# Optimization experiments

Measured on AMD Instinct MI355X. Metric: run time of the kernel, lower is better.

Reference implementation:

```python
import jax, jax.numpy as jnp
import numpy as np

NUM_HEADS = 8
EPS = 1e-12  # matches torch F.normalize eps


def setup_inputs() -> dict:
    key = jax.random.key(0)
    ks = jax.random.split(key, 4)
    B, C, H, W = 32, 384, 32, 32
    x = jax.random.normal(ks[0], (B, C, H, W), dtype=jnp.float32)
    w_qkv = jax.random.normal(ks[1], (3 * C, C), dtype=jnp.float32) * (1.0 / np.sqrt(C))
    b_qkv = jnp.zeros((3 * C,), dtype=jnp.float32)
    temperature = jnp.ones((NUM_HEADS, 1, 1), dtype=jnp.float32)
    w_proj = jax.random.normal(ks[2], (C, C), dtype=jnp.float32) * (1.0 / np.sqrt(C))
    b_proj = jnp.zeros((C,), dtype=jnp.float32)
    return {"x": x, "w_qkv": w_qkv, "b_qkv": b_qkv, "temperature": temperature,
            "w_proj": w_proj, "b_proj": b_proj}


def _l2norm_tokens(t):
    # L2-normalize over the token axis N (last dim), torch F.normalize semantics
    n = jnp.sqrt(jnp.sum(t * t, axis=-1, keepdims=True))
    return t / jnp.maximum(n, EPS)


def reference(x, w_qkv, b_qkv, temperature, w_proj, b_proj):
    B, C, H, W = x.shape
    N = H * W
    nh = NUM_HEADS
    dh = C // nh
    xf = x.reshape(B, C, N)
    # 1x1 conv == channel GEMM: [B,3C,N]
    qkv = jnp.einsum('oc,bcn->bon', w_qkv, xf) + b_qkv[:, None]
    qkv = qkv.reshape(B, 3, nh, dh, N)
    q, k, v = qkv[:, 0], qkv[:, 1], qkv[:, 2]  # each [B,nh,dh,N]
    q = _l2norm_tokens(q)
    k = _l2norm_tokens(k)
    # cross-covariance: contract over N -> small [B,nh,dh,dh]
    attn = jnp.einsum('bhdn,bhen->bhde', q, k) * temperature
    attn = jax.nn.softmax(attn, axis=-1)
    out = jnp.einsum('bhde,bhen->bhdn', attn, v).reshape(B, C, N)
    out = jnp.einsum('oc,bcn->bon', w_proj, out) + b_proj[:, None]
    return x + out.reshape(B, C, H, W)
```

## Files before the change

kernel.cpp:

```cpp
#include <hip/hip_runtime.h>
#include <hip/hip_bf16.h>
#include <stdint.h>

#define BATCH  32
#define CDIM   384
#define NTOK   1024
#define NHEADS 8
#define DH     48

using f32x4  = __attribute__((ext_vector_type(4))) float;
using bf16x8 = __attribute__((ext_vector_type(8))) short;
using u16x4  = __attribute__((ext_vector_type(4))) uint16_t;
using u16x8  = __attribute__((ext_vector_type(8))) uint16_t;

__device__ __forceinline__ uint16_t f2bf(float f) {
  uint32_t x = __float_as_uint(f);
  uint32_t r = (x + 0x7fffu + ((x >> 16) & 1u)) >> 16;
  return (uint16_t)r;
}
__device__ __forceinline__ float bf2f(uint16_t u) {
  return __uint_as_float(((uint32_t)u) << 16);
}

#define GLL16(gsrc, ldst)                                                    \
  __builtin_amdgcn_global_load_lds(                                          \
      (const __attribute__((address_space(1))) void*)(gsrc),                 \
      (__attribute__((address_space(3))) void*)(ldst), 16, 0, 0)

__global__ __launch_bounds__(256) void k_transpose_x(const float* __restrict__ x,
                                                     uint16_t* __restrict__ xT) {
  __shared__ float t[64][65];
  int tid = threadIdx.x;
  int n0 = blockIdx.x * 64;
  int c0 = blockIdx.y * 64;
  int b  = blockIdx.z;
  const float* xb = x + (size_t)b * CDIM * NTOK;
#pragma unroll
  for (int p = 0; p < 4; ++p) {
    int r  = (tid >> 4) + p * 16;
    int cc = (tid & 15) * 4;
    float4 v = *(const float4*)(xb + (size_t)(c0 + r) * NTOK + n0 + cc);
    t[r][cc + 0] = v.x; t[r][cc + 1] = v.y; t[r][cc + 2] = v.z; t[r][cc + 3] = v.w;
  }
  __syncthreads();
  uint16_t* xTb = xT + (size_t)b * NTOK * CDIM;
#pragma unroll
  for (int p = 0; p < 2; ++p) {
    int n  = (tid >> 3) + p * 32;
    int cb = (tid & 7) * 8;
    u16x8 o;
#pragma unroll
    for (int j = 0; j < 8; ++j) o[j] = f2bf(t[cb + j][n]);
    *(u16x8*)(xTb + (size_t)(n0 + n) * CDIM + c0 + cb) = o;
  }
}

__global__ __launch_bounds__(256) void k_convert_w(const float* __restrict__ wqkv,
                                                   const float* __restrict__ wproj,
                                                   uint16_t* __restrict__ wq,
                                                   uint16_t* __restrict__ wp) {
  int n1 = 3 * CDIM * CDIM;
  int n2 = CDIM * CDIM;
  int stride = gridDim.x * 256;
  for (int i = blockIdx.x * 256 + threadIdx.x; i < n1 + n2; i += stride) {
    if (i < n1) wq[i] = f2bf(wqkv[i]);
    else        wp[i - n1] = f2bf(wproj[i - n1]);
  }
}

__device__ __forceinline__ void gemm_tile_128(const uint16_t* __restrict__ A,
                                              const uint16_t* __restrict__ B,
                                              uint16_t* ldsA, uint16_t* ldsB,
                                              f32x4 acc[4][4], int tid) {
  const int K = 384;
  int w = tid >> 6, lane = tid & 63;
  int wr = w >> 1, wc = w & 1;
  int lr = lane & 15, g = lane >> 4;
  for (int kt = 0; kt < K; kt += 64) {
    __syncthreads();
#pragma unroll
    for (int iss = 0; iss < 4; ++iss) {
      int ch = tid + 256 * iss;
      int r  = ch >> 3;
      int cs = (((ch & 7) ^ (r & 7)) << 3);
      GLL16(A + (size_t)r * K + kt + cs, ldsA + (size_t)ch * 8);
      GLL16(B + (size_t)r * K + kt + cs, ldsB + (size_t)ch * 8);
    }
    __syncthreads();
#pragma unroll
    for (int ks = 0; ks < 2; ++ks) {
      bf16x8 af[4], bfr[4];
#pragma unroll
      for (int mt = 0; mt < 4; ++mt) {
        int row = wr * 64 + mt * 16 + lr;
        int sl  = (((ks * 4 + g) ^ (row & 7)) << 3);
        af[mt] = *(const bf16x8*)(ldsA + (size_t)row * 64 + sl);
      }
#pragma unroll
      for (int nt = 0; nt < 4; ++nt) {
        int row = wc * 64 + nt * 16 + lr;
        int sl  = (((ks * 4 + g) ^ (row & 7)) << 3);
        bfr[nt] = *(const bf16x8*)(ldsB + (size_t)row * 64 + sl);
      }
#pragma unroll
      for (int mt = 0; mt < 4; ++mt)
#pragma unroll
        for (int nt = 0; nt < 4; ++nt)
          acc[mt][nt] = __builtin_amdgcn_mfma_f32_16x16x32_bf16(af[mt], bfr[nt], acc[mt][nt], 0, 0, 0);
    }
  }
}

__global__ __launch_bounds__(256) void k_qkv(const uint16_t* __restrict__ Wq,
                                             const uint16_t* __restrict__ xT,
                                             const float* __restrict__ bqkv,
                                             uint16_t* __restrict__ qk,
                                             uint16_t* __restrict__ vT) {
  __shared__ uint16_t ldsA[128 * 64];
  __shared__ uint16_t ldsB[128 * 64];
  int tid = threadIdx.x;
  int id  = blockIdx.x;
  int xcd = id & 7, idx = id >> 3;
  int jt  = xcd * 32 + (idx & 31);
  int bm  = idx >> 5;
  int o0 = bm * 128, j0 = jt * 128;
  f32x4 acc[4][4];
#pragma unroll
  for (int i = 0; i < 4; ++i)
#pragma unroll
    for (int j = 0; j < 4; ++j) acc[i][j] = (f32x4){0.f, 0.f, 0.f, 0.f};

  gemm_tile_128(Wq + (size_t)o0 * 384, xT + (size_t)j0 * 384, ldsA, ldsB, acc, tid);

  int w = tid >> 6, lane = tid & 63;
  int wr = w >> 1, wc = w & 1, lr = lane & 15, g = lane >> 4;
#pragma unroll
  for (int mt = 0; mt < 4; ++mt) {
    int ob = o0 + wr * 64 + mt * 16 + g * 4;
    float b0 = bqkv[ob + 0], b1 = bqkv[ob + 1], b2 = bqkv[ob + 2], b3 = bqkv[ob + 3];
#pragma unroll
    for (int nt = 0; nt < 4; ++nt) {
      int j = j0 + wc * 64 + nt * 16 + lr;
      int b = j >> 10, n = j & 1023;
      f32x4 v = acc[mt][nt];
      float v0 = v[0] + b0, v1 = v[1] + b1, v2 = v[2] + b2, v3 = v[3] + b3;
      if (ob < 768) {
        uint16_t* dst = qk + ((size_t)(b * 768 + ob) * 1024 + n);
        dst[0] = f2bf(v0); dst[1024] = f2bf(v1); dst[2048] = f2bf(v2); dst[3072] = f2bf(v3);
      } else {
        int oc = ob - 768;
        int h = oc / 48, d = oc % 48;
        u16x4 p;
        p[0] = f2bf(v0); p[1] = f2bf(v1); p[2] = f2bf(v2); p[3] = f2bf(v3);
        *(u16x4*)(vT + ((size_t)((b * 8 + h) * 1024 + n) * 48 + d)) = p;
      }
    }
  }
}

__global__ __launch_bounds__(256) void k_attn(const uint16_t* __restrict__ qk,
                                              const uint16_t* __restrict__ vT,
                                              const float* __restrict__ temperature,
                                              uint16_t* __restrict__ aT) {
  __shared__ float Sp[4][48][49];
  __shared__ float Sf[48][49];
  __shared__ uint16_t P[48][72];
  __shared__ float nrm[96];
  int tid = threadIdx.x, w = tid >> 6, lane = tid & 63;
  int bh = blockIdx.x, b = bh >> 3, h = bh & 7;
  const uint16_t* qbase = qk + (size_t)(b * 768 + h * 48) * 1024;
  const uint16_t* kbase = qbase + (size_t)384 * 1024;

  for (int r = w; r < 96; r += 4) {
    const uint16_t* row = (r < 48) ? (qbase + (size_t)r * 1024)
                                   : (kbase + (size_t)(r - 48) * 1024);
    float s = 0.f;
#pragma unroll
    for (int jj = 0; jj < 4; ++jj) {
      u16x4 u = *(const u16x4*)(row + (size_t)(jj * 64 + lane) * 4);
#pragma unroll
      for (int e = 0; e < 4; ++e) { float f = bf2f(u[e]); s += f * f; }
    }
#pragma unroll
    for (int off = 32; off > 0; off >>= 1) s += __shfl_down(s, off);
    if (lane == 0) nrm[r] = fmaxf(sqrtf(s), 1e-12f);
  }

  int lr = lane & 15, g = lane >> 4;
  int nbase = w * 256;
  f32x4 sacc[3][3];
#pragma unroll
  for (int i = 0; i < 3; ++i)
#pragma unroll
    for (int j = 0; j < 3; ++j) sacc[i][j] = (f32x4){0.f, 0.f, 0.f, 0.f};
#pragma unroll
  for (int ks = 0; ks < 8; ++ks) {
    bf16x8 aq[3], bk[3];
#pragma unroll
    for (int mt = 0; mt < 3; ++mt)
      aq[mt] = *(const bf16x8*)(qbase + (size_t)(mt * 16 + lr) * 1024 + nbase + ks * 32 + g * 8);
#pragma unroll
    for (int et = 0; et < 3; ++et)
      bk[et] = *(const bf16x8*)(kbase + (size_t)(et * 16 + lr) * 1024 + nbase + ks * 32 + g * 8);
#pragma unroll
    for (int mt = 0; mt < 3; ++mt)
#pragma unroll
      for (int et = 0; et < 3; ++et)
        sacc[mt][et] = __builtin_amdgcn_mfma_f32_16x16x32_bf16(aq[mt], bk[et], sacc[mt][et], 0, 0, 0);
  }
#pragma unroll
  for (int mt = 0; mt < 3; ++mt)
#pragma unroll
    for (int et = 0; et < 3; ++et)
#pragma unroll
      for (int r = 0; r < 4; ++r)
        Sp[w][mt * 16 + g * 4 + r][et * 16 + lr] = sacc[mt][et][r];
  __syncthreads();

  float temp = temperature[h];
  for (int idx = tid; idx < 48 * 48; idx += 256) {
    int d = idx / 48, e = idx - d * 48;
    float s = Sp[0][d][e] + Sp[1][d][e] + Sp[2][d][e] + Sp[3][d][e];
    Sf[d][e] = s * temp / (nrm[d] * nrm[48 + e]);
  }
  __syncthreads();

  if (tid < 48) {
    int d = tid;
    float m = -1e30f;
    for (int e = 0; e < 48; ++e) m = fmaxf(m, Sf[d][e]);
    float sum = 0.f;
    for (int e = 0; e < 48; ++e) { float v = __expf(Sf[d][e] - m); sum += v; Sf[d][e] = v; }
    float inv = 1.f / sum;
    for (int e = 0; e < 48; ++e) P[d][e] = f2bf(Sf[d][e] * inv);
    for (int e = 48; e < 64; ++e) P[d][e] = 0;
  }
  __syncthreads();

  bf16x8 af[3][2];
#pragma unroll
  for (int mt = 0; mt < 3; ++mt)
#pragma unroll
    for (int ks = 0; ks < 2; ++ks)
      af[mt][ks] = *(const bf16x8*)(&P[mt * 16 + lr][ks * 32 + g * 8]);
  const uint16_t* vb = vT + (size_t)(b * 8 + h) * 1024 * 48;
  bf16x8 zf;
#pragma unroll
  for (int i = 0; i < 8; ++i) zf[i] = 0;
#pragma unroll 4
  for (int nt = 0; nt < 16; ++nt) {
    int n = w * 256 + nt * 16 + lr;
    bf16x8 bv[2];
    bv[0] = *(const bf16x8*)(vb + (size_t)n * 48 + g * 8);
    int eb1 = 32 + g * 8;
    bv[1] = (eb1 < 48) ? *(const bf16x8*)(vb + (size_t)n * 48 + eb1) : zf;
    f32x4 o[3];
#pragma unroll
    for (int mt = 0; mt < 3; ++mt) o[mt] = (f32x4){0.f, 0.f, 0.f, 0.f};
#pragma unroll
    for (int ks = 0; ks < 2; ++ks)
#pragma unroll
      for (int mt = 0; mt < 3; ++mt)
        o[mt] = __builtin_amdgcn_mfma_f32_16x16x32_bf16(af[mt][ks], bv[ks], o[mt], 0, 0, 0);
#pragma unroll
    for (int mt = 0; mt < 3; ++mt) {
      int c = h * 48 + mt * 16 + g * 4;
      u16x4 p;
#pragma unroll
      for (int r = 0; r < 4; ++r) p[r] = f2bf(o[mt][r]);
      *(u16x4*)(aT + ((size_t)(b * 1024 + n) * 384 + c)) = p;
    }
  }
}

__global__ __launch_bounds__(256) void k_proj(const uint16_t* __restrict__ Wp,
                                              const uint16_t* __restrict__ aT,
                                              const float* __restrict__ bproj,
                                              const float* __restrict__ x,
                                              float* __restrict__ out) {
  __shared__ uint16_t ldsA[128 * 64];
  __shared__ uint16_t ldsB[128 * 64];
  int tid = threadIdx.x;
  int id  = blockIdx.x;
  int xcd = id & 7, idx = id >> 3;
  int jt  = xcd * 32 + (idx & 31);
  int bm  = idx >> 5;
  int o0 = bm * 128, j0 = jt * 128;
  f32x4 acc[4][4];
#pragma unroll
  for (int i = 0; i < 4; ++i)
#pragma unroll
    for (int j = 0; j < 4; ++j) acc[i][j] = (f32x4){0.f, 0.f, 0.f, 0.f};

  gemm_tile_128(Wp + (size_t)o0 * 384, aT + (size_t)j0 * 384, ldsA, ldsB, acc, tid);

  int w = tid >> 6, lane = tid & 63;
  int wr = w >> 1, wc = w & 1, lr = lane & 15, g = lane >> 4;
#pragma unroll
  for (int mt = 0; mt < 4; ++mt) {
    int ob = o0 + wr * 64 + mt * 16 + g * 4;
    float b0 = bproj[ob + 0], b1 = bproj[ob + 1], b2 = bproj[ob + 2], b3 = bproj[ob + 3];
#pragma unroll
    for (int nt = 0; nt < 4; ++nt) {
      int j = j0 + wc * 64 + nt * 16 + lr;
      int b = j >> 10, n = j & 1023;
      f32x4 v = acc[mt][nt];
      size_t i0 = (size_t)(b * 384 + ob) * 1024 + n;
      out[i0]        = v[0] + b0 + x[i0];
      out[i0 + 1024] = v[1] + b1 + x[i0 + 1024];
      out[i0 + 2048] = v[2] + b2 + x[i0 + 2048];
      out[i0 + 3072] = v[3] + b3 + x[i0 + 3072];
    }
  }
}

extern "C" void kernel_launch(void* const* d_in, const int* in_sizes, int n_in,
                              void* d_out, int out_size, void* d_ws, size_t ws_size,
                              hipStream_t stream) {
  const float* x     = (const float*)d_in[0];
  const float* wqkv  = (const float*)d_in[1];
  const float* bqkv  = (const float*)d_in[2];
  const float* temp  = (const float*)d_in[3];
  const float* wproj = (const float*)d_in[4];
  const float* bproj = (const float*)d_in[5];
  float* out = (float*)d_out;

  char* ws = (char*)d_ws;
  size_t off = 0;
  auto alloc = [&](size_t bytes) -> char* {
    char* p = ws + off;
    off += (bytes + 255) & ~(size_t)255;
    return p;
  };
  uint16_t* xT    = (uint16_t*)alloc((size_t)BATCH * NTOK * CDIM * 2);
  uint16_t* wq_bf = (uint16_t*)alloc((size_t)3 * CDIM * CDIM * 2);
  uint16_t* wp_bf = (uint16_t*)alloc((size_t)CDIM * CDIM * 2);
  uint16_t* qkbuf = (uint16_t*)alloc((size_t)BATCH * 768 * NTOK * 2);
  uint16_t* vTbuf = (uint16_t*)alloc((size_t)BATCH * NHEADS * NTOK * DH * 2);
  uint16_t* aT    = xT;

  k_transpose_x<<<dim3(NTOK / 64, CDIM / 64, BATCH), dim3(256), 0, stream>>>(x, xT);
  k_convert_w<<<dim3(576), dim3(256), 0, stream>>>(wqkv, wproj, wq_bf, wp_bf);
  k_qkv<<<dim3(2304), dim3(256), 0, stream>>>(wq_bf, xT, bqkv, qkbuf, vTbuf);
  k_attn<<<dim3(256), dim3(256), 0, stream>>>(qkbuf, vTbuf, temp, aT);
  k_proj<<<dim3(768), dim3(256), 0, stream>>>(wp_bf, aT, bproj, x, out);
}
```

Before: 127.4 us.

## Fuse weight conversion into transpose, widen attention blocks, read bf16 residual

Folds the weight fp32-to-bf16 conversion into extra blocks of the transpose kernel, removing one launch. The attention kernel moves to 512-thread blocks, so each of 8 waves handles 128 tokens, raising parallelism per head. The transpose also writes a bf16 copy of x, and the projection epilogue reads this for the residual instead of fp32 x, halving that read. In exchange, the residual add loses precision and the transpose writes extra bytes.

```diff
diff --git a/kernel.cpp b/kernel.cpp
--- a/kernel.cpp
+++ b/kernel.cpp
@@ -28,19 +28,39 @@
       (__attribute__((address_space(3))) void*)(ldst), 16, 0, 0)
 
 __global__ __launch_bounds__(256) void k_transpose_x(const float* __restrict__ x,
-                                                     uint16_t* __restrict__ xT) {
+                                                     uint16_t* __restrict__ xT,
+                                                     uint16_t* __restrict__ xbf,
+                                                     int use_xbf,
+                                                     const float* __restrict__ wqkv,
+                                                     const float* __restrict__ wproj,
+                                                     uint16_t* __restrict__ wq,
+                                                     uint16_t* __restrict__ wp) {
+  int tid = threadIdx.x;
+  if (blockIdx.y == 6) {
+    int id = blockIdx.x + 16 * blockIdx.z;
+    int n1 = 3 * CDIM * CDIM, n2 = CDIM * CDIM;
+    for (int i = id * 256 + tid; i < n1 + n2; i += 512 * 256) {
+      if (i < n1) wq[i] = f2bf(wqkv[i]);
+      else        wp[i - n1] = f2bf(wproj[i - n1]);
+    }
+    return;
+  }
   __shared__ float t[64][65];
-  int tid = threadIdx.x;
   int n0 = blockIdx.x * 64;
   int c0 = blockIdx.y * 64;
   int b  = blockIdx.z;
   const float* xb = x + (size_t)b * CDIM * NTOK;
+  uint16_t* xbb = xbf + (size_t)b * CDIM * NTOK;
 #pragma unroll
   for (int p = 0; p < 4; ++p) {
     int r  = (tid >> 4) + p * 16;
     int cc = (tid & 15) * 4;
     float4 v = *(const float4*)(xb + (size_t)(c0 + r) * NTOK + n0 + cc);
     t[r][cc + 0] = v.x; t[r][cc + 1] = v.y; t[r][cc + 2] = v.z; t[r][cc + 3] = v.w;
+    if (use_xbf) {
+      u16x4 o; o[0] = f2bf(v.x); o[1] = f2bf(v.y); o[2] = f2bf(v.z); o[3] = f2bf(v.w);
+      *(u16x4*)(xbb + (size_t)(c0 + r) * NTOK + n0 + cc) = o;
+    }
   }
   __syncthreads();
   uint16_t* xTb = xT + (size_t)b * NTOK * CDIM;
@@ -52,19 +72,6 @@
 #pragma unroll
     for (int j = 0; j < 8; ++j) o[j] = f2bf(t[cb + j][n]);
     *(u16x8*)(xTb + (size_t)(n0 + n) * CDIM + c0 + cb) = o;
-  }
-}
-
-__global__ __launch_bounds__(256) void k_convert_w(const float* __restrict__ wqkv,
-                                                   const float* __restrict__ wproj,
-                                                   uint16_t* __restrict__ wq,
-                                                   uint16_t* __restrict__ wp) {
-  int n1 = 3 * CDIM * CDIM;
-  int n2 = CDIM * CDIM;
-  int stride = gridDim.x * 256;
-  for (int i = blockIdx.x * 256 + threadIdx.x; i < n1 + n2; i += stride) {
-    if (i < n1) wq[i] = f2bf(wqkv[i]);
-    else        wp[i - n1] = f2bf(wproj[i - n1]);
   }
 }
 
@@ -158,11 +165,11 @@
   }
 }
 
-__global__ __launch_bounds__(256) void k_attn(const uint16_t* __restrict__ qk,
+__global__ __launch_bounds__(512) void k_attn(const uint16_t* __restrict__ qk,
                                               const uint16_t* __restrict__ vT,
                                               const float* __restrict__ temperature,
                                               uint16_t* __restrict__ aT) {
-  __shared__ float Sp[4][48][49];
+  __shared__ float Sp[8][48][49];
   __shared__ float Sf[48][49];
   __shared__ uint16_t P[48][72];
   __shared__ float nrm[96];
@@ -171,7 +178,7 @@
   const uint16_t* qbase = qk + (size_t)(b * 768 + h * 48) * 1024;
   const uint16_t* kbase = qbase + (size_t)384 * 1024;
 
-  for (int r = w; r < 96; r += 4) {
+  for (int r = w; r < 96; r += 8) {
     const uint16_t* row = (r < 48) ? (qbase + (size_t)r * 1024)
                                    : (kbase + (size_t)(r - 48) * 1024);
     float s = 0.f;
@@ -187,14 +194,14 @@
   }
 
   int lr = lane & 15, g = lane >> 4;
-  int nbase = w * 256;
+  int nbase = w * 128;
   f32x4 sacc[3][3];
 #pragma unroll
   for (int i = 0; i < 3; ++i)
 #pragma unroll
     for (int j = 0; j < 3; ++j) sacc[i][j] = (f32x4){0.f, 0.f, 0.f, 0.f};
 #pragma unroll
-  for (int ks = 0; ks < 8; ++ks) {
+  for (int ks = 0; ks < 4; ++ks) {
     bf16x8 aq[3], bk[3];
 #pragma unroll
     for (int mt = 0; mt < 3; ++mt)
@@ -218,9 +225,11 @@
   __syncthreads();
 
   float temp = temperature[h];
-  for (int idx = tid; idx < 48 * 48; idx += 256) {
+  for (int idx = tid; idx < 48 * 48; idx += 512) {
     int d = idx / 48, e = idx - d * 48;
-    float s = Sp[0][d][e] + Sp[1][d][e] + Sp[2][d][e] + Sp[3][d][e];
+    float s = 0.f;
+#pragma unroll
+    for (int ww = 0; ww < 8; ++ww) s += Sp[ww][d][e];
     Sf[d][e] = s * temp / (nrm[d] * nrm[48 + e]);
   }
   __syncthreads();
@@ -247,9 +256,9 @@
   bf16x8 zf;
 #pragma unroll
   for (int i = 0; i < 8; ++i) zf[i] = 0;
-#pragma unroll 4
-  for (int nt = 0; nt < 16; ++nt) {
-    int n = w * 256 + nt * 16 + lr;
+#pragma unroll
+  for (int nt = 0; nt < 8; ++nt) {
+    int n = w * 128 + nt * 16 + lr;
     bf16x8 bv[2];
     bv[0] = *(const bf16x8*)(vb + (size_t)n * 48 + g * 8);
     int eb1 = 32 + g * 8;
@@ -276,8 +285,10 @@
 __global__ __launch_bounds__(256) void k_proj(const uint16_t* __restrict__ Wp,
                                               const uint16_t* __restrict__ aT,
                                               const float* __restrict__ bproj,
+                                              const uint16_t* __restrict__ xbf,
                                               const float* __restrict__ x,
-                                              float* __restrict__ out) {
+                                              float* __restrict__ out,
+                                              int use_xbf) {
   __shared__ uint16_t ldsA[128 * 64];
   __shared__ uint16_t ldsB[128 * 64];
   int tid = threadIdx.x;
@@ -306,10 +317,17 @@
       int b = j >> 10, n = j & 1023;
       f32x4 v = acc[mt][nt];
       size_t i0 = (size_t)(b * 384 + ob) * 1024 + n;
-      out[i0]        = v[0] + b0 + x[i0];
-      out[i0 + 1024] = v[1] + b1 + x[i0 + 1024];
-      out[i0 + 2048] = v[2] + b2 + x[i0 + 2048];
-      out[i0 + 3072] = v[3] + b3 + x[i0 + 3072];
+      float r0, r1, r2, r3;
+      if (use_xbf) {
+        r0 = bf2f(xbf[i0]); r1 = bf2f(xbf[i0 + 1024]);
+        r2 = bf2f(xbf[i0 + 2048]); r3 = bf2f(xbf[i0 + 3072]);
+      } else {
+        r0 = x[i0]; r1 = x[i0 + 1024]; r2 = x[i0 + 2048]; r3 = x[i0 + 3072];
+      }
+      out[i0]        = v[0] + b0 + r0;
+      out[i0 + 1024] = v[1] + b1 + r1;
+      out[i0 + 2048] = v[2] + b2 + r2;
+      out[i0 + 3072] = v[3] + b3 + r3;
     }
   }
 }
@@ -337,11 +355,14 @@
   uint16_t* wp_bf = (uint16_t*)alloc((size_t)CDIM * CDIM * 2);
   uint16_t* qkbuf = (uint16_t*)alloc((size_t)BATCH * 768 * NTOK * 2);
   uint16_t* vTbuf = (uint16_t*)alloc((size_t)BATCH * NHEADS * NTOK * DH * 2);
-  uint16_t* aT    = xT;
-
-  k_transpose_x<<<dim3(NTOK / 64, CDIM / 64, BATCH), dim3(256), 0, stream>>>(x, xT);
-  k_convert_w<<<dim3(576), dim3(256), 0, stream>>>(wqkv, wproj, wq_bf, wp_bf);
+  size_t xbf_bytes = (size_t)BATCH * CDIM * NTOK * 2;
+  int use_xbf = (off + xbf_bytes <= ws_size) ? 1 : 0;
+  uint16_t* xbf = use_xbf ? (uint16_t*)alloc(xbf_bytes) : (uint16_t*)xT;
+  uint16_t* aT  = xT;
+
+  k_transpose_x<<<dim3(NTOK / 64, 7, BATCH), dim3(256), 0, stream>>>(
+      x, xT, xbf, use_xbf, wqkv, wproj, wq_bf, wp_bf);
   k_qkv<<<dim3(2304), dim3(256), 0, stream>>>(wq_bf, xT, bqkv, qkbuf, vTbuf);
-  k_attn<<<dim3(256), dim3(256), 0, stream>>>(qkbuf, vTbuf, temp, aT);
-  k_proj<<<dim3(768), dim3(256), 0, stream>>>(wp_bf, aT, bproj, x, out);
-}
+  k_attn<<<dim3(256), dim3(512), 0, stream>>>(qkbuf, vTbuf, temp, aT);
+  k_proj<<<dim3(768), dim3(256), 0, stream>>>(wp_bf, aT, bproj, xbf, x, out, use_xbf);
+}
```

Result: no change. 125.3 us (-1.6%).
